# Kernel optimization log

Hardware: AMD Instinct MI355X
Metric: run time of the kernel (lower is better)

Reference implementation:

```python
import jax, jax.numpy as jnp
import numpy as np

B, SEQ, D_MODEL, N_HEADS = 4, 4096, 1024, 16
HEAD_DIM = D_MODEL // N_HEADS


def setup_inputs() -> dict:
    key = jax.random.key(0)
    ks = jax.random.split(key, 12)
    d = D_MODEL
    s = 1.0 / np.sqrt(d)  # ~nn.Linear init scale
    f = lambda k, shape, sc=1.0: jax.random.normal(k, shape, dtype=jnp.float32) * sc
    return {
        "queries": f(ks[0], (B, SEQ, d)),
        "keys":    f(ks[1], (B, SEQ, d)),
        "values":  f(ks[2], (B, SEQ, d)),
        "Wr": f(ks[3], (d, d), s), "br": jnp.zeros((d,), jnp.float32),
        "Wk": f(ks[4], (d, d), s), "bk": jnp.zeros((d,), jnp.float32),
        "Wv": f(ks[5], (d, d), s), "bv": jnp.zeros((d,), jnp.float32),
        "Wo": f(ks[6], (d, d), s), "bo": jnp.zeros((d,), jnp.float32),
        "decay": f(ks[7], (N_HEADS, HEAD_DIM), 0.01) - 5.0,
        "bonus": jnp.zeros((N_HEADS, HEAD_DIM), jnp.float32),
    }


def reference(queries, keys, values, Wr, br, Wk, bk, Wv, bv, Wo, bo, decay, bonus):
    Bb, N, d = queries.shape
    M = keys.shape[1]
    H = decay.shape[0]
    Dh = d // H

    # projections (nn.Linear: x @ W^T + b), split into heads
    r = (queries @ Wr.T + br).reshape(Bb, N, H, Dh)              # (B,N,H,D)
    k = (keys    @ Wk.T + bk).reshape(Bb, M, H, Dh).transpose(1, 0, 2, 3)  # (M,B,H,D)
    v = (values  @ Wv.T + bv).reshape(Bb, M, H, Dh).transpose(1, 0, 2, 3)  # (M,B,H,D)

    decay_factor = jnp.exp(-jnp.exp(decay))  # exp(w), w = -exp(decay); (H,D)

    def step(carry, kv):
        num, den = carry                       # (B,H,D)
        k_t, v_t = kv                          # (B,H,D)
        kc = jnp.clip(k_t, -10.0, 10.0)
        ek = jnp.exp(kc)
        bonus_w = jnp.exp(bonus + kc)          # (B,H,D) via broadcast
        wkv_t = (num + bonus_w * v_t) / (den + bonus_w + 1e-6)
        num = num * decay_factor + ek * v_t
        den = den * decay_factor + ek
        return (num, den), wkv_t

    init = (jnp.zeros((Bb, H, Dh), queries.dtype), jnp.zeros((Bb, H, Dh), queries.dtype))
    _, wkv = jax.lax.scan(step, init, (k, v))   # (M,B,H,D); here M == N
    wkv = wkv[:N].transpose(1, 0, 2, 3)         # (B,N,H,D)

    out = (jax.nn.sigmoid(r) * wkv).reshape(Bb, N, d)
    return out @ Wo.T + bo
```

## Files before the change

### kernel.cpp

```cpp
#include <hip/hip_runtime.h>

#define T_SEQ   4096
#define DM      1024
#define NB      4
#define ROWS    (NB * T_SEQ)
#define NCH     64
#define LCH     (T_SEQ / NCH)

typedef unsigned short ushort_t;

typedef __attribute__((ext_vector_type(8))) short bf16x8;
typedef __attribute__((ext_vector_type(4))) float f32x4;

__device__ __forceinline__ float bf2f(ushort_t u) {
  return __uint_as_float(((unsigned int)u) << 16);
}
__device__ __forceinline__ ushort_t f2bf(float f) {
  unsigned int u = __float_as_uint(f);
  u += 0x7FFFu + ((u >> 16) & 1u);
  return (ushort_t)(u >> 16);
}

__device__ __forceinline__ void async16(const void* g, void* l) {
  __builtin_amdgcn_global_load_lds(
      (const __attribute__((address_space(1))) unsigned int*)g,
      (__attribute__((address_space(3))) unsigned int*)l, 16, 0, 0);
}

__device__ __forceinline__ int fragoff(int row, int col) {
  int p = (((row >> 4) * 2 + (col >> 5)) << 10) + ((row & 15) << 6) + ((col & 31) << 1);
  return p ^ (((row >> 3) & 1) << 5);
}

__global__ __launch_bounds__(256)
void cvt_bf16(const float* __restrict__ in, ushort_t* __restrict__ out, const int n4) {
  const int stride = gridDim.x * blockDim.x;
  for (int i = blockIdx.x * blockDim.x + threadIdx.x; i < n4; i += stride) {
    const float4 f = ((const float4*)in)[i];
    ushort4 o;
    o.x = f2bf(f.x); o.y = f2bf(f.y); o.z = f2bf(f.z); o.w = f2bf(f.w);
    ((ushort4*)out)[i] = o;
  }
}

__device__ __forceinline__ void store_out(ushort_t* C, size_t i, float v) { C[i] = f2bf(v); }
__device__ __forceinline__ void store_out(float*    C, size_t i, float v) { C[i] = v; }

template <typename OutT>
__global__ __launch_bounds__(512, 2)
void gemm256(const ushort_t* __restrict__ A, const ushort_t* __restrict__ W,
             const float* __restrict__ bias, OutT* __restrict__ C,
             const int M, const int N, const int K) {
  __shared__ char smem[131072];
  const int T = K >> 6;
  const int nwg = (M >> 8) * (N >> 8);
  const int wg  = ((int)blockIdx.x & 7) * (nwg >> 3) + ((int)blockIdx.x >> 3);
  const int ntn = N >> 8;
  const int tm = wg / ntn, tn = wg % ntn;
  const int m0 = tm << 8, n0 = tn << 8;
  const int tid  = threadIdx.x;
  const int lane = tid & 63;
  const int wave = tid >> 6;
  const int wm128 = (wave >> 2) * 128;
  const int wn64  = (wave & 3) * 64;
  const int r15 = lane & 15;
  const int kq8 = (lane >> 4) * 8;

  int srow[2], scol[2];
  #pragma unroll
  for (int rho = 0; rho < 2; ++rho) {
    int p  = rho * 8192 + tid * 16;
    int pp = p ^ (((p >> 9) & 1) << 5);
    int e  = pp >> 1;
    int S = e >> 9, inr = e & 511;
    srow[rho] = ((S >> 1) << 4) + (inr >> 5);
    scol[rho] = ((S & 1) << 5) + (inr & 31);
  }

  auto stageA = [&](int tile, int half) {
    const int boff = ((tile & 1) << 15) + (half << 14);
    #pragma unroll
    for (int rho = 0; rho < 2; ++rho) {
      const ushort_t* g = A + (size_t)(m0 + half * 128 + srow[rho]) * K + (tile << 6) + scol[rho];
      async16(g, &smem[boff + rho * 8192 + tid * 16]);
    }
  };
  auto stageB = [&](int tile, int half) {
    const int boff = 65536 + ((tile & 1) << 15) + (half << 14);
    #pragma unroll
    for (int rho = 0; rho < 2; ++rho) {
      const ushort_t* g = W + (size_t)(n0 + half * 128 + srow[rho]) * K + (tile << 6) + scol[rho];
      async16(g, &smem[boff + rho * 8192 + tid * 16]);
    }
  };

  f32x4 acc[8][4];
  #pragma unroll
  for (int i = 0; i < 8; ++i)
    #pragma unroll
    for (int j = 0; j < 4; ++j)
      acc[i][j] = (f32x4){0.f, 0.f, 0.f, 0.f};
  bf16x8 bf[4][2];

  stageA(0, 0); stageA(0, 1); stageB(0, 0); stageB(0, 1); stageB(1, 0); stageB(1, 1);
  asm volatile("s_waitcnt vmcnt(4)" ::: "memory");
  __builtin_amdgcn_s_barrier();

#define GPHASE(Q, STG, TAILW)                                                    \
  {                                                                              \
    bf16x8 af[2][2];                                                             \
    _Pragma("unroll") for (int fl = 0; fl < 2; ++fl)                             \
      _Pragma("unroll") for (int ks = 0; ks < 2; ++ks)                           \
        af[fl][ks] = *(const bf16x8*)&smem[abase +                               \
            fragoff(wm128 + ((2 * (Q) + fl) << 4) + r15, (ks << 5) + kq8)];      \
    if ((Q) == 0) {                                                              \
      _Pragma("unroll") for (int fj = 0; fj < 4; ++fj)                           \
        _Pragma("unroll") for (int ks = 0; ks < 2; ++ks)                         \
          bf[fj][ks] = *(const bf16x8*)&smem[bbase +                             \
              fragoff(wn64 + (fj << 4) + r15, (ks << 5) + kq8)];                 \
    }                                                                            \
    STG();                                                                       \
    __builtin_amdgcn_s_barrier();                                                \
    __builtin_amdgcn_s_setprio(1);                                               \
    _Pragma("unroll") for (int fl = 0; fl < 2; ++fl)                             \
      _Pragma("unroll") for (int fj = 0; fj < 4; ++fj)                           \
        _Pragma("unroll") for (int ks = 0; ks < 2; ++ks)                         \
          acc[2 * (Q) + fl][fj] = __builtin_amdgcn_mfma_f32_16x16x32_bf16(       \
              af[fl][ks], bf[fj][ks], acc[2 * (Q) + fl][fj], 0, 0, 0);           \
    __builtin_amdgcn_s_setprio(0);                                               \
    TAILW();                                                                     \
    __builtin_amdgcn_s_barrier();                                                \
  }

  for (int j = 0; j < T; ++j) {
    const int abase = (j & 1) << 15;
    const int bbase = 65536 + ((j & 1) << 15);
    const bool p1 = (j + 1 < T), p2 = (j + 2 < T);
    auto stA0 = [&] { if (p1) stageA(j + 1, 0); };
    auto stA1 = [&] { if (p1) stageA(j + 1, 1); };
    auto stB0 = [&] { if (p2) stageB(j + 2, 0); };
    auto stB1 = [&] { if (p2) stageB(j + 2, 1); };
    auto nw   = [&] {};
    auto bwait = [&] {
      if (p2) asm volatile("s_waitcnt vmcnt(4)" ::: "memory");
      else    asm volatile("s_waitcnt vmcnt(0)" ::: "memory");
    };
    GPHASE(0, stA0, nw);
    GPHASE(1, stA1, nw);
    GPHASE(2, stB0, nw);
    GPHASE(3, stB1, bwait);
  }
#undef GPHASE

  float bias4[4];
  #pragma unroll
  for (int fj = 0; fj < 4; ++fj) bias4[fj] = bias[n0 + wn64 + fj * 16 + r15];
  #pragma unroll
  for (int fi = 0; fi < 8; ++fi) {
    const int row0 = m0 + wm128 + fi * 16 + (lane >> 4) * 4;
    #pragma unroll
    for (int fj = 0; fj < 4; ++fj) {
      const int col = n0 + wn64 + fj * 16 + r15;
      #pragma unroll
      for (int r = 0; r < 4; ++r)
        store_out(C, (size_t)(row0 + r) * N + col, acc[fi][fj][r] + bias4[fj]);
    }
  }
}

__global__ __launch_bounds__(256)
void wkv_pass1(const ushort_t* __restrict__ kp, const ushort_t* __restrict__ vp,
               const float* __restrict__ decay,
               float* __restrict__ s_num, float* __restrict__ s_den) {
  const int tid = threadIdx.x;
  const int grp = blockIdx.x & 3;
  const int c   = (blockIdx.x >> 2) & (NCH - 1);
  const int b   = (int)blockIdx.x >> 8;
  const int ch  = grp * 256 + tid;
  const float df = __expf(-__expf(decay[ch]));
  size_t idx = (size_t)b * T_SEQ * DM + (size_t)(c * LCH) * DM + ch;
  float num = 0.f, den = 0.f;
  for (int u = 0; u < LCH; ++u, idx += DM) {
    float kf = bf2f(kp[idx]);
    kf = fminf(fmaxf(kf, -10.f), 10.f);
    const float ek = __expf(kf);
    const float vv = bf2f(vp[idx]);
    num = fmaf(num, df, ek * vv);
    den = fmaf(den, df, ek);
  }
  const size_t si = ((size_t)b * NCH + c) * DM + ch;
  s_num[si] = num;
  s_den[si] = den;
}

__global__ __launch_bounds__(256)
void wkv_pass2(const float* __restrict__ decay,
               float* __restrict__ s_num, float* __restrict__ s_den) {
  const int tid = threadIdx.x;
  const int grp = blockIdx.x & 3;
  const int b   = (int)blockIdx.x >> 2;
  const int ch  = grp * 256 + tid;
  const float dfL = __expf(-__expf(decay[ch]) * (float)LCH);
  float an = 0.f, ad = 0.f;
  size_t si = (size_t)b * NCH * DM + ch;
  for (int c = 0; c < NCH; ++c, si += DM) {
    const float ln = s_num[si], ld = s_den[si];
    s_num[si] = an; s_den[si] = ad;
    an = fmaf(an, dfL, ln);
    ad = fmaf(ad, dfL, ld);
  }
}

__global__ __launch_bounds__(256)
void wkv_pass3(const ushort_t* __restrict__ kp, const ushort_t* __restrict__ vp,
               const ushort_t* __restrict__ rp, const float* __restrict__ decay,
               const float* __restrict__ bonus,
               const float* __restrict__ s_num, const float* __restrict__ s_den,
               ushort_t* __restrict__ G) {
  const int tid = threadIdx.x;
  const int grp = blockIdx.x & 3;
  const int c   = (blockIdx.x >> 2) & (NCH - 1);
  const int b   = (int)blockIdx.x >> 8;
  const int ch  = grp * 256 + tid;
  const float df = __expf(-__expf(decay[ch]));
  const float eb = __expf(bonus[ch]);
  const size_t si = ((size_t)b * NCH + c) * DM + ch;
  float num = s_num[si], den = s_den[si];
  size_t idx = (size_t)b * T_SEQ * DM + (size_t)(c * LCH) * DM + ch;
  for (int u = 0; u < LCH; ++u, idx += DM) {
    float kf = bf2f(kp[idx]);
    kf = fminf(fmaxf(kf, -10.f), 10.f);
    const float ek = __expf(kf);
    const float bw = eb * ek;
    const float vv = bf2f(vp[idx]);
    const float rr = bf2f(rp[idx]);
    const float numer = fmaf(bw, vv, num);
    const float denom = den + bw + 1e-6f;
    const float wkv = numer * __builtin_amdgcn_rcpf(denom);
    const float sig = __builtin_amdgcn_rcpf(1.f + __expf(-rr));
    G[idx] = f2bf(sig * wkv);
    num = fmaf(num, df, ek * vv);
    den = fmaf(den, df, ek);
  }
}

extern "C" void kernel_launch(void* const* d_in, const int* in_sizes, int n_in,
                              void* d_out, int out_size, void* d_ws, size_t ws_size,
                              hipStream_t stream) {
  const float* q   = (const float*)d_in[0];
  const float* ky  = (const float*)d_in[1];
  const float* vl  = (const float*)d_in[2];
  const float* Wr  = (const float*)d_in[3];
  const float* br  = (const float*)d_in[4];
  const float* Wk  = (const float*)d_in[5];
  const float* bk  = (const float*)d_in[6];
  const float* Wv  = (const float*)d_in[7];
  const float* bv  = (const float*)d_in[8];
  const float* Wo  = (const float*)d_in[9];
  const float* bo  = (const float*)d_in[10];
  const float* decay = (const float*)d_in[11];
  const float* bonus = (const float*)d_in[12];
  float* out = (float*)d_out;

  const size_t NE = (size_t)ROWS * DM;
  const size_t WE = (size_t)DM * DM;

  ushort_t* xb = (ushort_t*)d_ws;
  ushort_t* wb = xb + NE;
  ushort_t* rp = wb + WE;
  ushort_t* kp = rp + NE;
  ushort_t* vp = kp + NE;
  ushort_t* G  = xb;
  float* s_num = (float*)wb;
  float* s_den = s_num + (size_t)NB * NCH * DM;

  const int big4 = (int)(NE / 4);
  const int w4   = (int)(WE / 4);
  dim3 cB(256);
  dim3 gBig(2048), gW(1024);
  dim3 gemmGrid((ROWS / 256) * (DM / 256)), gemmBlk(512);
  dim3 scanGrid(NB * NCH * (DM / 256)), scanBlk(256);

  cvt_bf16<<<gBig, cB, 0, stream>>>(q, xb, big4);
  cvt_bf16<<<gW,   cB, 0, stream>>>(Wr, wb, w4);
  gemm256<ushort_t><<<gemmGrid, gemmBlk, 0, stream>>>(xb, wb, br, rp, ROWS, DM, DM);
  cvt_bf16<<<gBig, cB, 0, stream>>>(ky, xb, big4);
  cvt_bf16<<<gW,   cB, 0, stream>>>(Wk, wb, w4);
  gemm256<ushort_t><<<gemmGrid, gemmBlk, 0, stream>>>(xb, wb, bk, kp, ROWS, DM, DM);
  cvt_bf16<<<gBig, cB, 0, stream>>>(vl, xb, big4);
  cvt_bf16<<<gW,   cB, 0, stream>>>(Wv, wb, w4);
  gemm256<ushort_t><<<gemmGrid, gemmBlk, 0, stream>>>(xb, wb, bv, vp, ROWS, DM, DM);
  wkv_pass1<<<scanGrid, scanBlk, 0, stream>>>(kp, vp, decay, s_num, s_den);
  wkv_pass2<<<dim3(NB * DM / 256), scanBlk, 0, stream>>>(decay, s_num, s_den);
  wkv_pass3<<<scanGrid, scanBlk, 0, stream>>>(kp, vp, rp, decay, bonus, s_num, s_den, G);
  cvt_bf16<<<gW,   cB, 0, stream>>>(Wo, wb, w4);
  gemm256<float><<<gemmGrid, gemmBlk, 0, stream>>>(G, wb, bo, out, ROWS, DM, DM);
}
```

Measured before the change: 275.6 us.

## Fuse fp32-to-bf16 activation conversion into GEMM A loads and stage bf16 epilogue via LDS

The three projection GEMMs now read fp32 activations directly. Each tile is loaded into registers, converted to bf16 and written into the swizzled LDS layout, which removes the three separate large cvt_bf16 passes and their extra global traffic. The bf16-output epilogue also goes through LDS so each wave writes coalesced 16-byte row stores instead of scattered 2-byte stores. In exchange, A loading becomes synchronous register staging instead of async global-to-LDS copies, which raises register pressure and may weaken latency hiding in the pipelined loop.

```diff
diff --git a/kernel.cpp b/kernel.cpp
--- a/kernel.cpp
+++ b/kernel.cpp
@@ -43,14 +43,12 @@
   }
 }
 
-__device__ __forceinline__ void store_out(ushort_t* C, size_t i, float v) { C[i] = f2bf(v); }
-__device__ __forceinline__ void store_out(float*    C, size_t i, float v) { C[i] = v; }
-
-template <typename OutT>
+template <typename AT, typename OutT>
 __global__ __launch_bounds__(512, 2)
-void gemm256(const ushort_t* __restrict__ A, const ushort_t* __restrict__ W,
+void gemm256(const AT* __restrict__ A, const ushort_t* __restrict__ W,
              const float* __restrict__ bias, OutT* __restrict__ C,
              const int M, const int N, const int K) {
+  constexpr bool A_F32 = sizeof(AT) == 4;
   __shared__ char smem[131072];
   const int T = K >> 6;
   const int nwg = (M >> 8) * (N >> 8);
@@ -66,6 +64,9 @@
   const int r15 = lane & 15;
   const int kq8 = (lane >> 4) * 8;
 
+  const float*    Af = (const float*)A;
+  const ushort_t* Ab = (const ushort_t*)A;
+
   int srow[2], scol[2];
   #pragma unroll
   for (int rho = 0; rho < 2; ++rho) {
@@ -77,11 +78,11 @@
     scol[rho] = ((S & 1) << 5) + (inr & 31);
   }
 
-  auto stageA = [&](int tile, int half) {
+  auto stageAg = [&](int tile, int half) {
     const int boff = ((tile & 1) << 15) + (half << 14);
     #pragma unroll
     for (int rho = 0; rho < 2; ++rho) {
-      const ushort_t* g = A + (size_t)(m0 + half * 128 + srow[rho]) * K + (tile << 6) + scol[rho];
+      const ushort_t* g = Ab + (size_t)(m0 + half * 128 + srow[rho]) * K + (tile << 6) + scol[rho];
       async16(g, &smem[boff + rho * 8192 + tid * 16]);
     }
   };
@@ -94,6 +95,30 @@
     }
   };
 
+  float4 sA0[2][2], sA1[2][2];
+  auto loadA = [&](float4 (&s)[2][2], int tile, int half) {
+    #pragma unroll
+    for (int rho = 0; rho < 2; ++rho) {
+      const int rl = rho * 64 + (tid >> 3);
+      const float* g = Af + (size_t)(m0 + half * 128 + rl) * K + (tile << 6) + ((tid & 7) * 8);
+      s[rho][0] = *(const float4*)g;
+      s[rho][1] = *(const float4*)(g + 4);
+    }
+  };
+  auto writeA = [&](float4 (&s)[2][2], int tile, int half) {
+    const int boff = ((tile & 1) << 15) + (half << 14);
+    #pragma unroll
+    for (int rho = 0; rho < 2; ++rho) {
+      const int rl = rho * 64 + (tid >> 3);
+      uint4 w;
+      w.x = ((unsigned)f2bf(s[rho][0].y) << 16) | f2bf(s[rho][0].x);
+      w.y = ((unsigned)f2bf(s[rho][0].w) << 16) | f2bf(s[rho][0].z);
+      w.z = ((unsigned)f2bf(s[rho][1].y) << 16) | f2bf(s[rho][1].x);
+      w.w = ((unsigned)f2bf(s[rho][1].w) << 16) | f2bf(s[rho][1].z);
+      *(uint4*)&smem[boff + fragoff(rl, (tid & 7) * 8)] = w;
+    }
+  };
+
   f32x4 acc[8][4];
   #pragma unroll
   for (int i = 0; i < 8; ++i)
@@ -102,8 +127,17 @@
       acc[i][j] = (f32x4){0.f, 0.f, 0.f, 0.f};
   bf16x8 bf[4][2];
 
-  stageA(0, 0); stageA(0, 1); stageB(0, 0); stageB(0, 1); stageB(1, 0); stageB(1, 1);
-  asm volatile("s_waitcnt vmcnt(4)" ::: "memory");
+  if constexpr (A_F32) {
+    loadA(sA0, 0, 0); loadA(sA1, 0, 1);
+    stageB(0, 0); stageB(0, 1); stageB(1, 0); stageB(1, 1);
+    writeA(sA0, 0, 0); writeA(sA1, 0, 1);
+    asm volatile("s_waitcnt vmcnt(4)" ::: "memory");
+    asm volatile("s_waitcnt lgkmcnt(0)" ::: "memory");
+  } else {
+    stageAg(0, 0); stageAg(0, 1);
+    stageB(0, 0); stageB(0, 1); stageB(1, 0); stageB(1, 1);
+    asm volatile("s_waitcnt vmcnt(4)" ::: "memory");
+  }
   __builtin_amdgcn_s_barrier();
 
 #define GPHASE(Q, STG, TAILW)                                                    \
@@ -136,34 +170,68 @@
     const int abase = (j & 1) << 15;
     const int bbase = 65536 + ((j & 1) << 15);
     const bool p1 = (j + 1 < T), p2 = (j + 2 < T);
-    auto stA0 = [&] { if (p1) stageA(j + 1, 0); };
-    auto stA1 = [&] { if (p1) stageA(j + 1, 1); };
-    auto stB0 = [&] { if (p2) stageB(j + 2, 0); };
-    auto stB1 = [&] { if (p2) stageB(j + 2, 1); };
-    auto nw   = [&] {};
-    auto bwait = [&] {
-      if (p2) asm volatile("s_waitcnt vmcnt(4)" ::: "memory");
-      else    asm volatile("s_waitcnt vmcnt(0)" ::: "memory");
-    };
-    GPHASE(0, stA0, nw);
-    GPHASE(1, stA1, nw);
-    GPHASE(2, stB0, nw);
-    GPHASE(3, stB1, bwait);
+    auto nw = [&] {};
+    if constexpr (A_F32) {
+      auto s0 = [&] { if (p1) loadA(sA0, j + 1, 0); };
+      auto s1 = [&] { if (p1) { loadA(sA1, j + 1, 1); writeA(sA0, j + 1, 0); } };
+      auto s2 = [&] { if (p2) stageB(j + 2, 0); if (p1) writeA(sA1, j + 1, 1); };
+      auto s3 = [&] { if (p2) stageB(j + 2, 1); };
+      GPHASE(0, s0, nw);
+      GPHASE(1, s1, nw);
+      GPHASE(2, s2, nw);
+      GPHASE(3, s3, nw);
+    } else {
+      auto s0 = [&] { if (p1) stageAg(j + 1, 0); };
+      auto s1 = [&] { if (p1) stageAg(j + 1, 1); };
+      auto s2 = [&] { if (p2) stageB(j + 2, 0); };
+      auto s3 = [&] { if (p2) stageB(j + 2, 1); };
+      auto bwait = [&] {
+        if (p2) asm volatile("s_waitcnt vmcnt(4)" ::: "memory");
+        else    asm volatile("s_waitcnt vmcnt(0)" ::: "memory");
+      };
+      GPHASE(0, s0, nw);
+      GPHASE(1, s1, nw);
+      GPHASE(2, s2, nw);
+      GPHASE(3, s3, bwait);
+    }
   }
 #undef GPHASE
 
   float bias4[4];
   #pragma unroll
   for (int fj = 0; fj < 4; ++fj) bias4[fj] = bias[n0 + wn64 + fj * 16 + r15];
-  #pragma unroll
-  for (int fi = 0; fi < 8; ++fi) {
-    const int row0 = m0 + wm128 + fi * 16 + (lane >> 4) * 4;
-    #pragma unroll
-    for (int fj = 0; fj < 4; ++fj) {
-      const int col = n0 + wn64 + fj * 16 + r15;
+
+  if constexpr (sizeof(OutT) == 2) {
+    const int wbase = wave * 4096;
+    #pragma unroll
+    for (int fi = 0; fi < 8; ++fi) {
       #pragma unroll
-      for (int r = 0; r < 4; ++r)
-        store_out(C, (size_t)(row0 + r) * N + col, acc[fi][fj][r] + bias4[fj]);
+      for (int fj = 0; fj < 4; ++fj)
+        #pragma unroll
+        for (int r = 0; r < 4; ++r) {
+          const int row = (lane >> 4) * 4 + r;
+          const int col = fj * 16 + r15;
+          *(ushort_t*)&smem[wbase + (row * 64 + col) * 2] = f2bf(acc[fi][fj][r] + bias4[fj]);
+        }
+      #pragma unroll
+      for (int round = 0; round < 2; ++round) {
+        const uint4 q = *(const uint4*)&smem[wbase + round * 1024 + lane * 16];
+        const int rl   = round * 8 + (lane >> 3);
+        const int col8 = (lane & 7) * 8;
+        *(uint4*)&C[(size_t)(m0 + wm128 + fi * 16 + rl) * N + n0 + wn64 + col8] = q;
+      }
+    }
+  } else {
+    #pragma unroll
+    for (int fi = 0; fi < 8; ++fi) {
+      const int row0 = m0 + wm128 + fi * 16 + (lane >> 4) * 4;
+      #pragma unroll
+      for (int fj = 0; fj < 4; ++fj) {
+        const int col = n0 + wn64 + fj * 16 + r15;
+        #pragma unroll
+        for (int r = 0; r < 4; ++r)
+          C[(size_t)(row0 + r) * N + col] = acc[fi][fj][r] + bias4[fj];
+      }
     }
   }
 }
@@ -274,25 +342,20 @@
   float* s_num = (float*)wb;
   float* s_den = s_num + (size_t)NB * NCH * DM;
 
-  const int big4 = (int)(NE / 4);
-  const int w4   = (int)(WE / 4);
-  dim3 cB(256);
-  dim3 gBig(2048), gW(1024);
+  const int w4 = (int)(WE / 4);
+  dim3 cB(256), gW(1024);
   dim3 gemmGrid((ROWS / 256) * (DM / 256)), gemmBlk(512);
   dim3 scanGrid(NB * NCH * (DM / 256)), scanBlk(256);
 
-  cvt_bf16<<<gBig, cB, 0, stream>>>(q, xb, big4);
-  cvt_bf16<<<gW,   cB, 0, stream>>>(Wr, wb, w4);
-  gemm256<ushort_t><<<gemmGrid, gemmBlk, 0, stream>>>(xb, wb, br, rp, ROWS, DM, DM);
-  cvt_bf16<<<gBig, cB, 0, stream>>>(ky, xb, big4);
-  cvt_bf16<<<gW,   cB, 0, stream>>>(Wk, wb, w4);
-  gemm256<ushort_t><<<gemmGrid, gemmBlk, 0, stream>>>(xb, wb, bk, kp, ROWS, DM, DM);
-  cvt_bf16<<<gBig, cB, 0, stream>>>(vl, xb, big4);
-  cvt_bf16<<<gW,   cB, 0, stream>>>(Wv, wb, w4);
-  gemm256<ushort_t><<<gemmGrid, gemmBlk, 0, stream>>>(xb, wb, bv, vp, ROWS, DM, DM);
+  cvt_bf16<<<gW, cB, 0, stream>>>(Wr, wb, w4);
+  gemm256<float, ushort_t><<<gemmGrid, gemmBlk, 0, stream>>>(q, wb, br, rp, ROWS, DM, DM);
+  cvt_bf16<<<gW, cB, 0, stream>>>(Wk, wb, w4);
+  gemm256<float, ushort_t><<<gemmGrid, gemmBlk, 0, stream>>>(ky, wb, bk, kp, ROWS, DM, DM);
+  cvt_bf16<<<gW, cB, 0, stream>>>(Wv, wb, w4);
+  gemm256<float, ushort_t><<<gemmGrid, gemmBlk, 0, stream>>>(vl, wb, bv, vp, ROWS, DM, DM);
   wkv_pass1<<<scanGrid, scanBlk, 0, stream>>>(kp, vp, decay, s_num, s_den);
   wkv_pass2<<<dim3(NB * DM / 256), scanBlk, 0, stream>>>(decay, s_num, s_den);
   wkv_pass3<<<scanGrid, scanBlk, 0, stream>>>(kp, vp, rp, decay, bonus, s_num, s_den, G);
-  cvt_bf16<<<gW,   cB, 0, stream>>>(Wo, wb, w4);
-  gemm256<float><<<gemmGrid, gemmBlk, 0, stream>>>(G, wb, bo, out, ROWS, DM, DM);
-}
+  cvt_bf16<<<gW, cB, 0, stream>>>(Wo, wb, w4);
+  gemm256<ushort_t, float><<<gemmGrid, gemmBlk, 0, stream>>>(G, wb, bo, out, ROWS, DM, DM);
+}
```

New measurement: 392.1 us. 42.3% more time.

## Fuse fp32-to-bf16 activation conversion into a single batched QKV projection GEMM

Applied to the files above, without the earlier changes.

Removes the three large activation cvt_bf16 passes. A new projection GEMM stages fp32 activation tiles directly into LDS with a K=32 tile and converts them to bf16 with v_cvt_pk_bf16_f32 while building fragments. The three projections are batched into one launch over a 3x grid, and the weight/bias conversion is packed into one kernel. wkv_pass3 writes its gated output in place over r, which saves workspace. The trade-offs are doubled LDS traffic for fp32 A tiles, a smaller K tile that adds more barriers per K step, and conversion work inside the GEMM loop.

```diff
diff --git a/kernel.cpp b/kernel.cpp
--- a/kernel.cpp
+++ b/kernel.cpp
@@ -20,6 +20,11 @@
   u += 0x7FFFu + ((u >> 16) & 1u);
   return (ushort_t)(u >> 16);
 }
+__device__ __forceinline__ unsigned cvtpk(float lo, float hi) {
+  unsigned r;
+  asm("v_cvt_pk_bf16_f32 %0, %1, %2" : "=v"(r) : "v"(lo), "v"(hi));
+  return r;
+}
 
 __device__ __forceinline__ void async16(const void* g, void* l) {
   __builtin_amdgcn_global_load_lds(
@@ -31,20 +36,38 @@
   int p = (((row >> 4) * 2 + (col >> 5)) << 10) + ((row & 15) << 6) + ((col & 31) << 1);
   return p ^ (((row >> 3) & 1) << 5);
 }
+__device__ __forceinline__ int fragoffB32(int row, int col) {
+  int p = ((row >> 4) << 10) + ((row & 15) << 6) + (col << 1);
+  return p ^ (((row >> 3) & 1) << 5);
+}
+__device__ __forceinline__ int fragoffA32f(int row, int col) {
+  int p = ((row >> 3) << 10) + ((row & 7) << 7) + (col << 2);
+  return p ^ ((row & 7) << 4);
+}
 
 __global__ __launch_bounds__(256)
-void cvt_bf16(const float* __restrict__ in, ushort_t* __restrict__ out, const int n4) {
-  const int stride = gridDim.x * blockDim.x;
-  for (int i = blockIdx.x * blockDim.x + threadIdx.x; i < n4; i += stride) {
-    const float4 f = ((const float4*)in)[i];
-    ushort4 o;
-    o.x = f2bf(f.x); o.y = f2bf(f.y); o.z = f2bf(f.z); o.w = f2bf(f.w);
-    ((ushort4*)out)[i] = o;
-  }
-}
-
-__device__ __forceinline__ void store_out(ushort_t* C, size_t i, float v) { C[i] = f2bf(v); }
-__device__ __forceinline__ void store_out(float*    C, size_t i, float v) { C[i] = v; }
+void cvt_pack(const float* __restrict__ Wr, const float* __restrict__ Wk,
+              const float* __restrict__ Wv, const float* __restrict__ Wo,
+              const float* __restrict__ br, const float* __restrict__ bk,
+              const float* __restrict__ bv, const float* __restrict__ bo,
+              ushort_t* __restrict__ wb, float* __restrict__ biasP) {
+  const int bid = blockIdx.x;
+  if (bid < 2048) {
+    const int n4 = (DM * DM);
+    for (int i = bid * 256 + threadIdx.x; i < n4; i += 2048 * 256) {
+      const int seg = i >> 18;
+      const float* src = seg == 0 ? Wr : seg == 1 ? Wk : seg == 2 ? Wv : Wo;
+      const float4 f = ((const float4*)src)[i & 262143];
+      ushort4 o;
+      o.x = f2bf(f.x); o.y = f2bf(f.y); o.z = f2bf(f.z); o.w = f2bf(f.w);
+      ((ushort4*)wb)[i] = o;
+    }
+  } else {
+    const int s = bid - 2048;
+    const float* b = s == 0 ? br : s == 1 ? bk : s == 2 ? bv : bo;
+    for (int i = threadIdx.x; i < DM; i += 256) biasP[s * DM + i] = b[i];
+  }
+}
 
 template <typename OutT>
 __global__ __launch_bounds__(512, 2)
@@ -136,21 +159,161 @@
     const int abase = (j & 1) << 15;
     const int bbase = 65536 + ((j & 1) << 15);
     const bool p1 = (j + 1 < T), p2 = (j + 2 < T);
-    auto stA0 = [&] { if (p1) stageA(j + 1, 0); };
-    auto stA1 = [&] { if (p1) stageA(j + 1, 1); };
-    auto stB0 = [&] { if (p2) stageB(j + 2, 0); };
-    auto stB1 = [&] { if (p2) stageB(j + 2, 1); };
-    auto nw   = [&] {};
+    auto s0 = [&] { if (p1) stageA(j + 1, 0); };
+    auto s1 = [&] { if (p1) stageA(j + 1, 1); };
+    auto s2 = [&] { if (p2) stageB(j + 2, 0); };
+    auto s3 = [&] { if (p2) stageB(j + 2, 1); };
+    auto nw = [&] {};
     auto bwait = [&] {
       if (p2) asm volatile("s_waitcnt vmcnt(4)" ::: "memory");
       else    asm volatile("s_waitcnt vmcnt(0)" ::: "memory");
     };
-    GPHASE(0, stA0, nw);
-    GPHASE(1, stA1, nw);
-    GPHASE(2, stB0, nw);
-    GPHASE(3, stB1, bwait);
+    GPHASE(0, s0, nw);
+    GPHASE(1, s1, nw);
+    GPHASE(2, s2, nw);
+    GPHASE(3, s3, bwait);
   }
 #undef GPHASE
+
+  float bias4[4];
+  #pragma unroll
+  for (int fj = 0; fj < 4; ++fj) bias4[fj] = bias[n0 + wn64 + fj * 16 + r15];
+  #pragma unroll
+  for (int fi = 0; fi < 8; ++fi) {
+    const int row0 = m0 + wm128 + fi * 16 + (lane >> 4) * 4;
+    #pragma unroll
+    for (int fj = 0; fj < 4; ++fj) {
+      const int col = n0 + wn64 + fj * 16 + r15;
+      #pragma unroll
+      for (int r = 0; r < 4; ++r) {
+        const float v = acc[fi][fj][r] + bias4[fj];
+        if constexpr (sizeof(OutT) == 2) C[(size_t)(row0 + r) * N + col] = f2bf(v);
+        else                             C[(size_t)(row0 + r) * N + col] = v;
+      }
+    }
+  }
+}
+
+__global__ __launch_bounds__(512, 2)
+void gemm256_proj(const float* __restrict__ Aq, const float* __restrict__ Ak,
+                  const float* __restrict__ Av, const ushort_t* __restrict__ Wb,
+                  const float* __restrict__ biasP, ushort_t* __restrict__ Cb,
+                  const int M, const int N, const int K) {
+  __shared__ char smem[98304];
+  const int T = K >> 5;
+  const int wg = ((int)blockIdx.x & 7) * 96 + ((int)blockIdx.x >> 3);
+  const int g  = wg >> 8;
+  const int local = wg & 255;
+  const int ntn = N >> 8;
+  const int tm = local / ntn, tn = local % ntn;
+  const int m0 = tm << 8, n0 = tn << 8;
+  const float*    Af = g == 0 ? Aq : (g == 1 ? Ak : Av);
+  const ushort_t* W  = Wb + (size_t)g * N * K;
+  const float*  bias = biasP + g * N;
+  ushort_t*        C = Cb + (size_t)g * M * N;
+
+  const int tid  = threadIdx.x;
+  const int lane = tid & 63;
+  const int wave = tid >> 6;
+  const int wm128 = (wave >> 2) * 128;
+  const int wn64  = (wave & 3) * 64;
+  const int r15 = lane & 15;
+  const int kq8 = (lane >> 4) * 8;
+
+  int arow[2], acol[2];
+  #pragma unroll
+  for (int rho = 0; rho < 2; ++rho) {
+    const int p = rho * 8192 + tid * 16;
+    const int e = p ^ (((p >> 7) & 7) << 4);
+    arow[rho] = ((p >> 10) << 3) | ((p >> 7) & 7);
+    acol[rho] = (e >> 2) & 31;
+  }
+  int brow, bcol;
+  {
+    const int p = tid * 16;
+    const int pp = p ^ (((p >> 9) & 1) << 5);
+    const int e = pp >> 1;
+    brow = ((e >> 9) << 4) | ((e >> 5) & 15);
+    bcol = e & 31;
+  }
+
+  auto stageA = [&](int tile, int half) {
+    const int boff = ((tile & 1) << 15) + (half << 14);
+    #pragma unroll
+    for (int rho = 0; rho < 2; ++rho) {
+      const float* g2 = Af + (size_t)(m0 + half * 128 + arow[rho]) * K + (tile << 5) + acol[rho];
+      async16(g2, &smem[boff + rho * 8192 + tid * 16]);
+    }
+  };
+  auto stageB = [&](int tile, int half) {
+    const int boff = 65536 + ((tile & 1) << 14) + (half << 13);
+    const ushort_t* g2 = W + (size_t)(n0 + half * 128 + brow) * K + (tile << 5) + bcol;
+    async16(g2, &smem[boff + tid * 16]);
+  };
+
+  auto rdA = [&](int abase, int row) -> bf16x8 {
+    const int adlo = abase + fragoffA32f(row, kq8);
+    const int adhi = abase + fragoffA32f(row, kq8 + 4);
+    const f32x4 lo = *(const f32x4*)&smem[adlo];
+    const f32x4 hi = *(const f32x4*)&smem[adhi];
+    union { uint4 u4; bf16x8 b; } cv;
+    cv.u4.x = cvtpk(lo[0], lo[1]); cv.u4.y = cvtpk(lo[2], lo[3]);
+    cv.u4.z = cvtpk(hi[0], hi[1]); cv.u4.w = cvtpk(hi[2], hi[3]);
+    return cv.b;
+  };
+
+  f32x4 acc[8][4];
+  #pragma unroll
+  for (int i = 0; i < 8; ++i)
+    #pragma unroll
+    for (int j = 0; j < 4; ++j)
+      acc[i][j] = (f32x4){0.f, 0.f, 0.f, 0.f};
+  bf16x8 bf[4];
+
+  stageA(0, 0); stageA(0, 1); stageB(0, 0); stageB(0, 1); stageB(1, 0); stageB(1, 1);
+  asm volatile("s_waitcnt vmcnt(2)" ::: "memory");
+  __builtin_amdgcn_s_barrier();
+
+#define PPHASE(Q, STG, TAILW)                                                    \
+  {                                                                              \
+    bf16x8 af[2];                                                                \
+    _Pragma("unroll") for (int fl = 0; fl < 2; ++fl)                             \
+      af[fl] = rdA(abase, wm128 + ((2 * (Q) + fl) << 4) + r15);                  \
+    if ((Q) == 0) {                                                              \
+      _Pragma("unroll") for (int fj = 0; fj < 4; ++fj)                           \
+        bf[fj] = *(const bf16x8*)&smem[bbase +                                   \
+            fragoffB32(wn64 + (fj << 4) + r15, kq8)];                            \
+    }                                                                            \
+    STG();                                                                       \
+    __builtin_amdgcn_s_barrier();                                                \
+    __builtin_amdgcn_s_setprio(1);                                               \
+    _Pragma("unroll") for (int fl = 0; fl < 2; ++fl)                             \
+      _Pragma("unroll") for (int fj = 0; fj < 4; ++fj)                           \
+        acc[2 * (Q) + fl][fj] = __builtin_amdgcn_mfma_f32_16x16x32_bf16(         \
+            af[fl], bf[fj], acc[2 * (Q) + fl][fj], 0, 0, 0);                     \
+    __builtin_amdgcn_s_setprio(0);                                               \
+    TAILW();                                                                     \
+    __builtin_amdgcn_s_barrier();                                                \
+  }
+
+  for (int j = 0; j < T; ++j) {
+    const int abase = (j & 1) << 15;
+    const int bbase = 65536 + ((j & 1) << 14);
+    const bool p1 = (j + 1 < T), p2 = (j + 2 < T);
+    auto s0 = [&] { if (p1) stageA(j + 1, 0); };
+    auto s1 = [&] { if (p1) stageA(j + 1, 1); };
+    auto s2 = [&] { if (p2) { stageB(j + 2, 0); stageB(j + 2, 1); } };
+    auto nw = [&] {};
+    auto bwait = [&] {
+      if (p2) asm volatile("s_waitcnt vmcnt(2)" ::: "memory");
+      else    asm volatile("s_waitcnt vmcnt(0)" ::: "memory");
+    };
+    PPHASE(0, s0, nw);
+    PPHASE(1, s1, nw);
+    PPHASE(2, s2, nw);
+    PPHASE(3, nw, bwait);
+  }
+#undef PPHASE
 
   float bias4[4];
   #pragma unroll
@@ -163,7 +326,7 @@
       const int col = n0 + wn64 + fj * 16 + r15;
       #pragma unroll
       for (int r = 0; r < 4; ++r)
-        store_out(C, (size_t)(row0 + r) * N + col, acc[fi][fj][r] + bias4[fj]);
+        C[(size_t)(row0 + r) * N + col] = f2bf(acc[fi][fj][r] + bias4[fj]);
     }
   }
 }
@@ -213,10 +376,9 @@
 
 __global__ __launch_bounds__(256)
 void wkv_pass3(const ushort_t* __restrict__ kp, const ushort_t* __restrict__ vp,
-               const ushort_t* __restrict__ rp, const float* __restrict__ decay,
+               ushort_t* rg, const float* __restrict__ decay,
                const float* __restrict__ bonus,
-               const float* __restrict__ s_num, const float* __restrict__ s_den,
-               ushort_t* __restrict__ G) {
+               const float* __restrict__ s_num, const float* __restrict__ s_den) {
   const int tid = threadIdx.x;
   const int grp = blockIdx.x & 3;
   const int c   = (blockIdx.x >> 2) & (NCH - 1);
@@ -233,12 +395,12 @@
     const float ek = __expf(kf);
     const float bw = eb * ek;
     const float vv = bf2f(vp[idx]);
-    const float rr = bf2f(rp[idx]);
+    const float rr = bf2f(rg[idx]);
     const float numer = fmaf(bw, vv, num);
     const float denom = den + bw + 1e-6f;
     const float wkv = numer * __builtin_amdgcn_rcpf(denom);
     const float sig = __builtin_amdgcn_rcpf(1.f + __expf(-rr));
-    G[idx] = f2bf(sig * wkv);
+    rg[idx] = f2bf(sig * wkv);
     num = fmaf(num, df, ek * vv);
     den = fmaf(den, df, ek);
   }
@@ -265,34 +427,24 @@
   const size_t NE = (size_t)ROWS * DM;
   const size_t WE = (size_t)DM * DM;
 
-  ushort_t* xb = (ushort_t*)d_ws;
-  ushort_t* wb = xb + NE;
-  ushort_t* rp = wb + WE;
+  ushort_t* wb = (ushort_t*)d_ws;
+  float* biasP = (float*)(wb + 4 * WE);
+  ushort_t* rp = (ushort_t*)(biasP + 4 * DM);
   ushort_t* kp = rp + NE;
   ushort_t* vp = kp + NE;
-  ushort_t* G  = xb;
-  float* s_num = (float*)wb;
+  float* s_num = (float*)(vp + NE);
   float* s_den = s_num + (size_t)NB * NCH * DM;
-
-  const int big4 = (int)(NE / 4);
-  const int w4   = (int)(WE / 4);
+  ushort_t* G  = rp;
+
   dim3 cB(256);
-  dim3 gBig(2048), gW(1024);
   dim3 gemmGrid((ROWS / 256) * (DM / 256)), gemmBlk(512);
+  dim3 projGrid(3 * (ROWS / 256) * (DM / 256));
   dim3 scanGrid(NB * NCH * (DM / 256)), scanBlk(256);
 
-  cvt_bf16<<<gBig, cB, 0, stream>>>(q, xb, big4);
-  cvt_bf16<<<gW,   cB, 0, stream>>>(Wr, wb, w4);
-  gemm256<ushort_t><<<gemmGrid, gemmBlk, 0, stream>>>(xb, wb, br, rp, ROWS, DM, DM);
-  cvt_bf16<<<gBig, cB, 0, stream>>>(ky, xb, big4);
-  cvt_bf16<<<gW,   cB, 0, stream>>>(Wk, wb, w4);
-  gemm256<ushort_t><<<gemmGrid, gemmBlk, 0, stream>>>(xb, wb, bk, kp, ROWS, DM, DM);
-  cvt_bf16<<<gBig, cB, 0, stream>>>(vl, xb, big4);
-  cvt_bf16<<<gW,   cB, 0, stream>>>(Wv, wb, w4);
-  gemm256<ushort_t><<<gemmGrid, gemmBlk, 0, stream>>>(xb, wb, bv, vp, ROWS, DM, DM);
+  cvt_pack<<<dim3(2052), cB, 0, stream>>>(Wr, Wk, Wv, Wo, br, bk, bv, bo, wb, biasP);
+  gemm256_proj<<<projGrid, gemmBlk, 0, stream>>>(q, ky, vl, wb, biasP, rp, ROWS, DM, DM);
   wkv_pass1<<<scanGrid, scanBlk, 0, stream>>>(kp, vp, decay, s_num, s_den);
   wkv_pass2<<<dim3(NB * DM / 256), scanBlk, 0, stream>>>(decay, s_num, s_den);
-  wkv_pass3<<<scanGrid, scanBlk, 0, stream>>>(kp, vp, rp, decay, bonus, s_num, s_den, G);
-  cvt_bf16<<<gW,   cB, 0, stream>>>(Wo, wb, w4);
-  gemm256<float><<<gemmGrid, gemmBlk, 0, stream>>>(G, wb, bo, out, ROWS, DM, DM);
-}
+  wkv_pass3<<<scanGrid, scanBlk, 0, stream>>>(kp, vp, rp, decay, bonus, s_num, s_den);
+  gemm256<float><<<gemmGrid, gemmBlk, 0, stream>>>(G, wb + 3 * WE, biasP + 3 * DM, out, ROWS, DM, DM);
+}
```

New measurement: 258.8 us. 6.1% less time.

## Fuse fp32-to-bf16 conversion into GEMM loads and batch three projections in one launch

Applied to the files above, without the earlier changes.

The projection GEMM now loads fp32 activations straight into LDS and converts them to bf16 while reading fragments, so the separate activation conversion passes and their global round trip go away. The three Q/K/V projections run as one batched launch, and all weights and biases are converted in a single packing kernel. The GEMM is retuned to K-tiles of 32 with triple buffering, and the output GEMM reads the gated result in place. The fp32 A tile doubles LDS traffic and per-fragment conversion work inside the GEMM main loop, and the 96KB of LDS may limit overlap.

```diff
diff --git a/kernel.cpp b/kernel.cpp
--- a/kernel.cpp
+++ b/kernel.cpp
@@ -20,6 +20,11 @@
   u += 0x7FFFu + ((u >> 16) & 1u);
   return (ushort_t)(u >> 16);
 }
+__device__ __forceinline__ unsigned cvtpk(float lo, float hi) {
+  unsigned r;
+  asm("v_cvt_pk_bf16_f32 %0, %1, %2" : "=v"(r) : "v"(lo), "v"(hi));
+  return r;
+}
 
 __device__ __forceinline__ void async16(const void* g, void* l) {
   __builtin_amdgcn_global_load_lds(
@@ -27,37 +32,65 @@
       (__attribute__((address_space(3))) unsigned int*)l, 16, 0, 0);
 }
 
-__device__ __forceinline__ int fragoff(int row, int col) {
-  int p = (((row >> 4) * 2 + (col >> 5)) << 10) + ((row & 15) << 6) + ((col & 31) << 1);
+__device__ __forceinline__ int fragoffB32(int row, int col) {
+  int p = ((row >> 4) << 10) + ((row & 15) << 6) + (col << 1);
   return p ^ (((row >> 3) & 1) << 5);
 }
+__device__ __forceinline__ int fragoffA32f(int row, int col) {
+  int p = ((row >> 3) << 10) + ((row & 7) << 7) + (col << 2);
+  return p ^ ((row & 7) << 4);
+}
 
 __global__ __launch_bounds__(256)
-void cvt_bf16(const float* __restrict__ in, ushort_t* __restrict__ out, const int n4) {
-  const int stride = gridDim.x * blockDim.x;
-  for (int i = blockIdx.x * blockDim.x + threadIdx.x; i < n4; i += stride) {
-    const float4 f = ((const float4*)in)[i];
-    ushort4 o;
-    o.x = f2bf(f.x); o.y = f2bf(f.y); o.z = f2bf(f.z); o.w = f2bf(f.w);
-    ((ushort4*)out)[i] = o;
-  }
-}
-
-__device__ __forceinline__ void store_out(ushort_t* C, size_t i, float v) { C[i] = f2bf(v); }
-__device__ __forceinline__ void store_out(float*    C, size_t i, float v) { C[i] = v; }
-
-template <typename OutT>
+void cvt_pack(const float* __restrict__ Wr, const float* __restrict__ Wk,
+              const float* __restrict__ Wv, const float* __restrict__ Wo,
+              const float* __restrict__ br, const float* __restrict__ bk,
+              const float* __restrict__ bv, const float* __restrict__ bo,
+              ushort_t* __restrict__ wb, float* __restrict__ biasP) {
+  const int bid = blockIdx.x;
+  if (bid < 2048) {
+    const int n4 = (DM * DM);
+    for (int i = bid * 256 + threadIdx.x; i < n4; i += 2048 * 256) {
+      const int seg = i >> 18;
+      const float* src = seg == 0 ? Wr : seg == 1 ? Wk : seg == 2 ? Wv : Wo;
+      const float4 f = ((const float4*)src)[i & 262143];
+      ushort4 o;
+      o.x = f2bf(f.x); o.y = f2bf(f.y); o.z = f2bf(f.z); o.w = f2bf(f.w);
+      ((ushort4*)wb)[i] = o;
+    }
+  } else {
+    const int s = bid - 2048;
+    const float* b = s == 0 ? br : s == 1 ? bk : s == 2 ? bv : bo;
+    for (int i = threadIdx.x; i < DM; i += 256) biasP[s * DM + i] = b[i];
+  }
+}
+
+template <typename AT, typename OutT, int GROUPS>
 __global__ __launch_bounds__(512, 2)
-void gemm256(const ushort_t* __restrict__ A, const ushort_t* __restrict__ W,
-             const float* __restrict__ bias, OutT* __restrict__ C,
-             const int M, const int N, const int K) {
-  __shared__ char smem[131072];
-  const int T = K >> 6;
-  const int nwg = (M >> 8) * (N >> 8);
-  const int wg  = ((int)blockIdx.x & 7) * (nwg >> 3) + ((int)blockIdx.x >> 3);
+void gemm3(const AT* __restrict__ A0, const AT* __restrict__ A1,
+           const AT* __restrict__ A2, const ushort_t* __restrict__ Wb,
+           const float* __restrict__ biasP, OutT* __restrict__ Cb,
+           const int M, const int N, const int K) {
+  constexpr bool A_F32 = sizeof(AT) == 4;
+  constexpr int ABYTES = A_F32 ? 32768 : 16384;
+  constexpr int BBYTES = 16384;
+  constexpr int AL = A_F32 ? 4 : 2;
+  __shared__ char smem[3 * (ABYTES + BBYTES)];
+
+  const int T = K >> 5;
+  const int ntpg = (M >> 8) * (N >> 8);
+  const int nwg  = GROUPS * ntpg;
+  const int wg   = ((int)blockIdx.x & 7) * (nwg >> 3) + ((int)blockIdx.x >> 3);
+  const int g     = wg / ntpg;
+  const int local = wg % ntpg;
   const int ntn = N >> 8;
-  const int tm = wg / ntn, tn = wg % ntn;
+  const int tm = local / ntn, tn = local % ntn;
   const int m0 = tm << 8, n0 = tn << 8;
+  const AT*       Ag   = g == 0 ? A0 : (g == 1 ? A1 : A2);
+  const ushort_t* W    = Wb + (size_t)g * N * K;
+  const float*    bias = biasP + g * N;
+  OutT*           C    = Cb + (size_t)g * M * N;
+
   const int tid  = threadIdx.x;
   const int lane = tid & 63;
   const int wave = tid >> 6;
@@ -66,31 +99,55 @@
   const int r15 = lane & 15;
   const int kq8 = (lane >> 4) * 8;
 
-  int srow[2], scol[2];
+  int arow[AL], acol[AL];
+  #pragma unroll
+  for (int rho = 0; rho < AL; ++rho) {
+    const int p = rho * 8192 + tid * 16;
+    if constexpr (A_F32) {
+      arow[rho] = ((p >> 10) << 3) | ((p >> 7) & 7);
+      acol[rho] = ((p ^ (((p >> 7) & 7) << 4)) >> 2) & 31;
+    } else {
+      const int e = (p ^ (((p >> 9) & 1) << 5)) >> 1;
+      arow[rho] = ((e >> 9) << 4) | ((e >> 5) & 15);
+      acol[rho] = e & 31;
+    }
+  }
+  int brow[2], bcol[2];
   #pragma unroll
   for (int rho = 0; rho < 2; ++rho) {
-    int p  = rho * 8192 + tid * 16;
-    int pp = p ^ (((p >> 9) & 1) << 5);
-    int e  = pp >> 1;
-    int S = e >> 9, inr = e & 511;
-    srow[rho] = ((S >> 1) << 4) + (inr >> 5);
-    scol[rho] = ((S & 1) << 5) + (inr & 31);
-  }
-
-  auto stageA = [&](int tile, int half) {
-    const int boff = ((tile & 1) << 15) + (half << 14);
+    const int p = rho * 8192 + tid * 16;
+    const int e = (p ^ (((p >> 9) & 1) << 5)) >> 1;
+    brow[rho] = ((e >> 9) << 4) | ((e >> 5) & 15);
+    bcol[rho] = e & 31;
+  }
+
+  auto stageA = [&](int tile) {
+    const int boff = (tile % 3) * ABYTES;
+    #pragma unroll
+    for (int rho = 0; rho < AL; ++rho) {
+      const AT* g2 = Ag + (size_t)(m0 + arow[rho]) * K + (tile << 5) + acol[rho];
+      async16(g2, &smem[boff + rho * 8192 + tid * 16]);
+    }
+  };
+  auto stageB = [&](int tile) {
+    const int boff = 3 * ABYTES + (tile % 3) * BBYTES;
     #pragma unroll
     for (int rho = 0; rho < 2; ++rho) {
-      const ushort_t* g = A + (size_t)(m0 + half * 128 + srow[rho]) * K + (tile << 6) + scol[rho];
-      async16(g, &smem[boff + rho * 8192 + tid * 16]);
+      const ushort_t* g2 = W + (size_t)(n0 + brow[rho]) * K + (tile << 5) + bcol[rho];
+      async16(g2, &smem[boff + rho * 8192 + tid * 16]);
     }
   };
-  auto stageB = [&](int tile, int half) {
-    const int boff = 65536 + ((tile & 1) << 15) + (half << 14);
-    #pragma unroll
-    for (int rho = 0; rho < 2; ++rho) {
-      const ushort_t* g = W + (size_t)(n0 + half * 128 + srow[rho]) * K + (tile << 6) + scol[rho];
-      async16(g, &smem[boff + rho * 8192 + tid * 16]);
+
+  auto rdAfrag = [&](int abase, int row) -> bf16x8 {
+    if constexpr (A_F32) {
+      const f32x4 lo = *(const f32x4*)&smem[abase + fragoffA32f(row, kq8)];
+      const f32x4 hi = *(const f32x4*)&smem[abase + fragoffA32f(row, kq8 + 4)];
+      union { uint4 u4; bf16x8 b; } cv;
+      cv.u4.x = cvtpk(lo[0], lo[1]); cv.u4.y = cvtpk(lo[2], lo[3]);
+      cv.u4.z = cvtpk(hi[0], hi[1]); cv.u4.w = cvtpk(hi[2], hi[3]);
+      return cv.b;
+    } else {
+      return *(const bf16x8*)&smem[abase + fragoffB32(row, kq8)];
     }
   };
 
@@ -100,57 +157,55 @@
     #pragma unroll
     for (int j = 0; j < 4; ++j)
       acc[i][j] = (f32x4){0.f, 0.f, 0.f, 0.f};
-  bf16x8 bf[4][2];
-
-  stageA(0, 0); stageA(0, 1); stageB(0, 0); stageB(0, 1); stageB(1, 0); stageB(1, 1);
-  asm volatile("s_waitcnt vmcnt(4)" ::: "memory");
+  bf16x8 bfr[4];
+
+  stageA(0); stageB(0); stageA(1); stageB(1);
+  if constexpr (A_F32) asm volatile("s_waitcnt vmcnt(6)" ::: "memory");
+  else                 asm volatile("s_waitcnt vmcnt(4)" ::: "memory");
   __builtin_amdgcn_s_barrier();
 
-#define GPHASE(Q, STG, TAILW)                                                    \
+#define PH3(H, STG, TAILW)                                                       \
   {                                                                              \
-    bf16x8 af[2][2];                                                             \
-    _Pragma("unroll") for (int fl = 0; fl < 2; ++fl)                             \
-      _Pragma("unroll") for (int ks = 0; ks < 2; ++ks)                           \
-        af[fl][ks] = *(const bf16x8*)&smem[abase +                               \
-            fragoff(wm128 + ((2 * (Q) + fl) << 4) + r15, (ks << 5) + kq8)];      \
-    if ((Q) == 0) {                                                              \
+    bf16x8 af[4];                                                                \
+    _Pragma("unroll") for (int q = 0; q < 4; ++q)                                \
+      af[q] = rdAfrag(curA, wm128 + (H) * 64 + q * 16 + r15);                    \
+    if ((H) == 0) {                                                              \
       _Pragma("unroll") for (int fj = 0; fj < 4; ++fj)                           \
-        _Pragma("unroll") for (int ks = 0; ks < 2; ++ks)                         \
-          bf[fj][ks] = *(const bf16x8*)&smem[bbase +                             \
-              fragoff(wn64 + (fj << 4) + r15, (ks << 5) + kq8)];                 \
+        bfr[fj] = *(const bf16x8*)&smem[curB +                                   \
+            fragoffB32(wn64 + (fj << 4) + r15, kq8)];                            \
     }                                                                            \
     STG();                                                                       \
     __builtin_amdgcn_s_barrier();                                                \
     __builtin_amdgcn_s_setprio(1);                                               \
-    _Pragma("unroll") for (int fl = 0; fl < 2; ++fl)                             \
+    _Pragma("unroll") for (int q = 0; q < 4; ++q)                                \
       _Pragma("unroll") for (int fj = 0; fj < 4; ++fj)                           \
-        _Pragma("unroll") for (int ks = 0; ks < 2; ++ks)                         \
-          acc[2 * (Q) + fl][fj] = __builtin_amdgcn_mfma_f32_16x16x32_bf16(       \
-              af[fl][ks], bf[fj][ks], acc[2 * (Q) + fl][fj], 0, 0, 0);           \
+        acc[(H) * 4 + q][fj] = __builtin_amdgcn_mfma_f32_16x16x32_bf16(          \
+            af[q], bfr[fj], acc[(H) * 4 + q][fj], 0, 0, 0);                      \
     __builtin_amdgcn_s_setprio(0);                                               \
     TAILW();                                                                     \
     __builtin_amdgcn_s_barrier();                                                \
   }
 
   for (int j = 0; j < T; ++j) {
-    const int abase = (j & 1) << 15;
-    const int bbase = 65536 + ((j & 1) << 15);
+    const int curA = (j % 3) * ABYTES;
+    const int curB = 3 * ABYTES + (j % 3) * BBYTES;
     const bool p1 = (j + 1 < T), p2 = (j + 2 < T);
-    auto stA0 = [&] { if (p1) stageA(j + 1, 0); };
-    auto stA1 = [&] { if (p1) stageA(j + 1, 1); };
-    auto stB0 = [&] { if (p2) stageB(j + 2, 0); };
-    auto stB1 = [&] { if (p2) stageB(j + 2, 1); };
-    auto nw   = [&] {};
-    auto bwait = [&] {
-      if (p2) asm volatile("s_waitcnt vmcnt(4)" ::: "memory");
-      else    asm volatile("s_waitcnt vmcnt(0)" ::: "memory");
+    auto sA = [&] { if (p2) stageA(j + 2); };
+    auto sB = [&] { if (p2) stageB(j + 2); };
+    auto nw = [&] {};
+    auto tw = [&] {
+      if (!p1) return;
+      if (p2) {
+        if constexpr (A_F32) asm volatile("s_waitcnt vmcnt(6)" ::: "memory");
+        else                 asm volatile("s_waitcnt vmcnt(4)" ::: "memory");
+      } else {
+        asm volatile("s_waitcnt vmcnt(0)" ::: "memory");
+      }
     };
-    GPHASE(0, stA0, nw);
-    GPHASE(1, stA1, nw);
-    GPHASE(2, stB0, nw);
-    GPHASE(3, stB1, bwait);
-  }
-#undef GPHASE
+    PH3(0, sA, nw);
+    PH3(1, sB, tw);
+  }
+#undef PH3
 
   float bias4[4];
   #pragma unroll
@@ -162,8 +217,11 @@
     for (int fj = 0; fj < 4; ++fj) {
       const int col = n0 + wn64 + fj * 16 + r15;
       #pragma unroll
-      for (int r = 0; r < 4; ++r)
-        store_out(C, (size_t)(row0 + r) * N + col, acc[fi][fj][r] + bias4[fj]);
+      for (int r = 0; r < 4; ++r) {
+        const float v = acc[fi][fj][r] + bias4[fj];
+        if constexpr (sizeof(OutT) == 2) C[(size_t)(row0 + r) * N + col] = f2bf(v);
+        else                             C[(size_t)(row0 + r) * N + col] = v;
+      }
     }
   }
 }
@@ -213,10 +271,9 @@
 
 __global__ __launch_bounds__(256)
 void wkv_pass3(const ushort_t* __restrict__ kp, const ushort_t* __restrict__ vp,
-               const ushort_t* __restrict__ rp, const float* __restrict__ decay,
+               ushort_t* rg, const float* __restrict__ decay,
                const float* __restrict__ bonus,
-               const float* __restrict__ s_num, const float* __restrict__ s_den,
-               ushort_t* __restrict__ G) {
+               const float* __restrict__ s_num, const float* __restrict__ s_den) {
   const int tid = threadIdx.x;
   const int grp = blockIdx.x & 3;
   const int c   = (blockIdx.x >> 2) & (NCH - 1);
@@ -233,12 +290,12 @@
     const float ek = __expf(kf);
     const float bw = eb * ek;
     const float vv = bf2f(vp[idx]);
-    const float rr = bf2f(rp[idx]);
+    const float rr = bf2f(rg[idx]);
     const float numer = fmaf(bw, vv, num);
     const float denom = den + bw + 1e-6f;
     const float wkv = numer * __builtin_amdgcn_rcpf(denom);
     const float sig = __builtin_amdgcn_rcpf(1.f + __expf(-rr));
-    G[idx] = f2bf(sig * wkv);
+    rg[idx] = f2bf(sig * wkv);
     num = fmaf(num, df, ek * vv);
     den = fmaf(den, df, ek);
   }
@@ -265,34 +322,27 @@
   const size_t NE = (size_t)ROWS * DM;
   const size_t WE = (size_t)DM * DM;
 
-  ushort_t* xb = (ushort_t*)d_ws;
-  ushort_t* wb = xb + NE;
-  ushort_t* rp = wb + WE;
+  ushort_t* wb = (ushort_t*)d_ws;
+  float* biasP = (float*)(wb + 4 * WE);
+  ushort_t* rp = (ushort_t*)(biasP + 4 * DM);
   ushort_t* kp = rp + NE;
   ushort_t* vp = kp + NE;
-  ushort_t* G  = xb;
-  float* s_num = (float*)wb;
+  float* s_num = (float*)(vp + NE);
   float* s_den = s_num + (size_t)NB * NCH * DM;
-
-  const int big4 = (int)(NE / 4);
-  const int w4   = (int)(WE / 4);
+  ushort_t* G  = rp;
+
   dim3 cB(256);
-  dim3 gBig(2048), gW(1024);
-  dim3 gemmGrid((ROWS / 256) * (DM / 256)), gemmBlk(512);
+  dim3 gemmBlk(512);
+  dim3 projGrid(3 * (ROWS / 256) * (DM / 256));
+  dim3 gemmGrid((ROWS / 256) * (DM / 256));
   dim3 scanGrid(NB * NCH * (DM / 256)), scanBlk(256);
 
-  cvt_bf16<<<gBig, cB, 0, stream>>>(q, xb, big4);
-  cvt_bf16<<<gW,   cB, 0, stream>>>(Wr, wb, w4);
-  gemm256<ushort_t><<<gemmGrid, gemmBlk, 0, stream>>>(xb, wb, br, rp, ROWS, DM, DM);
-  cvt_bf16<<<gBig, cB, 0, stream>>>(ky, xb, big4);
-  cvt_bf16<<<gW,   cB, 0, stream>>>(Wk, wb, w4);
-  gemm256<ushort_t><<<gemmGrid, gemmBlk, 0, stream>>>(xb, wb, bk, kp, ROWS, DM, DM);
-  cvt_bf16<<<gBig, cB, 0, stream>>>(vl, xb, big4);
-  cvt_bf16<<<gW,   cB, 0, stream>>>(Wv, wb, w4);
-  gemm256<ushort_t><<<gemmGrid, gemmBlk, 0, stream>>>(xb, wb, bv, vp, ROWS, DM, DM);
+  cvt_pack<<<dim3(2052), cB, 0, stream>>>(Wr, Wk, Wv, Wo, br, bk, bv, bo, wb, biasP);
+  gemm3<float, ushort_t, 3><<<projGrid, gemmBlk, 0, stream>>>(
+      q, ky, vl, wb, biasP, rp, ROWS, DM, DM);
   wkv_pass1<<<scanGrid, scanBlk, 0, stream>>>(kp, vp, decay, s_num, s_den);
   wkv_pass2<<<dim3(NB * DM / 256), scanBlk, 0, stream>>>(decay, s_num, s_den);
-  wkv_pass3<<<scanGrid, scanBlk, 0, stream>>>(kp, vp, rp, decay, bonus, s_num, s_den, G);
-  cvt_bf16<<<gW,   cB, 0, stream>>>(Wo, wb, w4);
-  gemm256<float><<<gemmGrid, gemmBlk, 0, stream>>>(G, wb, bo, out, ROWS, DM, DM);
-}
+  wkv_pass3<<<scanGrid, scanBlk, 0, stream>>>(kp, vp, rp, decay, bonus, s_num, s_den);
+  gemm3<ushort_t, float, 1><<<gemmGrid, gemmBlk, 0, stream>>>(
+      G, G, G, wb + 3 * WE, biasP + 3 * DM, out, ROWS, DM, DM);
+}
```

Measured after the change: 254.4 us. 7.7% less time.
